# Kernel tuning notes

Hardware: AMD Instinct MI355X
Metric: run time of the kernel (lower is better)

The kernel has to match this reference:

```python
import jax, jax.numpy as jnp
import numpy as np


def setup_inputs() -> dict:
    key = jax.random.key(0)
    ks = jax.random.split(key, 8)
    B, H, W, C = 4, 64, 64, 64
    d = C // 8
    x = jax.random.normal(ks[0], (B, H, W, C), dtype=jnp.float32)
    # 1x1 conv kernels (spectral-normalized in the original; here we use the
    # already-normalized weight matrices directly, scaled to unit-ish norm)
    Wf = jax.random.normal(ks[1], (C, d), dtype=jnp.float32) * (1.0 / np.sqrt(C))
    bf = jnp.zeros((d,), dtype=jnp.float32)
    Wg = jax.random.normal(ks[2], (C, d), dtype=jnp.float32) * (1.0 / np.sqrt(C))
    bg = jnp.zeros((d,), dtype=jnp.float32)
    Wh = jax.random.normal(ks[3], (C, C), dtype=jnp.float32) * (1.0 / np.sqrt(C))
    bh = jnp.zeros((C,), dtype=jnp.float32)
    gamma = jnp.float32(1.0)
    return {"x": x, "Wf": Wf, "bf": bf, "Wg": Wg, "bg": bg,
            "Wh": Wh, "bh": bh, "gamma": gamma}


def reference(x, Wf, bf, Wg, bg, Wh, bh, gamma):
    # x: [B, H, W, C] (NHWC, as Keras Conv2D default)
    B, H, W, C = x.shape
    N = H * W
    # 1x1 convs == per-pixel channel matmuls
    q = jnp.einsum('bhwc,cd->bhwd', x, Wf) + bf   # [B,H,W,C//8]
    k = jnp.einsum('bhwc,cd->bhwd', x, Wg) + bg   # [B,H,W,C//8]
    v = jnp.einsum('bhwc,cd->bhwd', x, Wh) + bh   # [B,H,W,C]
    q = q.reshape(B, N, -1)
    k = k.reshape(B, N, -1)
    v = v.reshape(B, N, C)
    # full non-causal attention (no 1/sqrt(d) scaling in the original)
    s = jnp.einsum('bnd,bmd->bnm', q, k)          # [B,N,N]
    s = jax.nn.softmax(s, axis=-1)
    o = jnp.einsum('bnm,bmc->bnc', s, v)          # [B,N,C]
    o = o.reshape(B, H, W, C)
    return gamma * o + x
```

## Files before the change

### kernel.cpp

```cpp
#include <hip/hip_runtime.h>
#include <hip/hip_bf16.h>

#define BATCH 4
#define NTOK 4096
#define CCH 64
#define KSPLIT 2
#define KPB (NTOK / KSPLIT)
#define NTILE (KPB / 64)
#define TPW (NTILE / 4)

#define QSCALE 184.66496523f
#define SBIAS  16251.0f

typedef short s16x8 __attribute__((ext_vector_type(8)));
typedef float f32x4 __attribute__((ext_vector_type(4)));

static __device__ __forceinline__ unsigned short f2bf(float f) {
    union { __hip_bfloat16 h; unsigned short u; } cv;
    cv.h = __float2bfloat16(f);
    return cv.u;
}
static __device__ __forceinline__ float bf2f(unsigned short u) {
    union { unsigned int u; float f; } c; c.u = ((unsigned)u) << 16;
    return c.f;
}
static __device__ __forceinline__ float bf_split(float f, unsigned short& h) {
    h = f2bf(f);
    return f - bf2f(h);
}
static __device__ __forceinline__ unsigned pack_rne(float a, float b) {
    return ((unsigned)f2bf(b) << 16) | f2bf(a);
}
static __device__ __forceinline__ unsigned pack_bits(float a, float b) {
    return ((unsigned)(int)b << 16) | (unsigned)(int)a;
}

__global__ __launch_bounds__(256) void proj_kernel(
    const float* __restrict__ xg,
    const float* __restrict__ Wf, const float* __restrict__ bf_,
    const float* __restrict__ Wg, const float* __restrict__ bg,
    const float* __restrict__ Wh, const float* __restrict__ bh,
    unsigned short* __restrict__ Qp, unsigned short* __restrict__ Kp,
    unsigned short* __restrict__ vTg)
{
    __shared__ float xS[32 * 68];
    __shared__ unsigned short xbS[32 * 72];
    __shared__ float WfT[8 * 68];
    __shared__ float WgT[8 * 68];
    __shared__ unsigned short vtS[64 * 40];

    const int t = threadIdx.x;
    const int b = blockIdx.x >> 7;
    const int n0 = (blockIdx.x & 127) * 32;

    const float* xrow = xg + ((size_t)b * NTOK + n0) * CCH;
    for (int f = t; f < 512; f += 256) {
        int r = f >> 4, c4 = (f & 15) * 4;
        float4 v = *(const float4*)(xrow + r * 64 + c4);
        *(float4*)(xS + r * 68 + c4) = v;
        uint2 pk = { pack_rne(v.x, v.y), pack_rne(v.z, v.w) };
        *(uint2*)(xbS + r * 72 + c4) = pk;
    }
    for (int e = t; e < 512; e += 256) {
        int ci = e >> 3, j = e & 7;
        WfT[j * 68 + ci] = Wf[e];
        WgT[j * 68 + ci] = Wg[e];
    }
    __syncthreads();

    const int w = t >> 6, lane = t & 63, ml = lane & 15, quad = lane >> 4;

    {
        s16x8 a0, a1;
        #pragma unroll
        for (int j = 0; j < 8; ++j) {
            a0[j] = (short)f2bf(Wh[(quad * 8 + j) * 64 + w * 16 + ml]);
            a1[j] = (short)f2bf(Wh[(32 + quad * 8 + j) * 64 + w * 16 + ml]);
        }
        #pragma unroll
        for (int nf = 0; nf < 2; ++nf) {
            int tok = nf * 16 + ml;
            s16x8 b0 = *(const s16x8*)(xbS + tok * 72 + quad * 8);
            s16x8 b1 = *(const s16x8*)(xbS + tok * 72 + 32 + quad * 8);
            f32x4 cc = __builtin_amdgcn_mfma_f32_16x16x32_bf16(a0, b0, (f32x4){0.f,0.f,0.f,0.f}, 0, 0, 0);
            cc = __builtin_amdgcn_mfma_f32_16x16x32_bf16(a1, b1, cc, 0, 0, 0);
            #pragma unroll
            for (int reg = 0; reg < 4; ++reg) {
                int cout = w * 16 + quad * 4 + reg;
                vtS[cout * 40 + nf * 16 + ml] = f2bf(cc[reg] + bh[cout]);
            }
        }
    }

    {
        int r = t >> 3, j = t & 7;
        float q = bf_[j], k = bg[j];
        for (int ci = 0; ci < 64; ci += 4) {
            float4 x4 = *(const float4*)(xS + r * 68 + ci);
            float4 wf4 = *(const float4*)(WfT + j * 68 + ci);
            float4 wg4 = *(const float4*)(WgT + j * 68 + ci);
            q += x4.x * wf4.x + x4.y * wf4.y + x4.z * wf4.z + x4.w * wf4.w;
            k += x4.x * wg4.x + x4.y * wg4.y + x4.z * wg4.z + x4.w * wg4.w;
        }
        q *= QSCALE;
        unsigned short qh, kh;
        float qres = bf_split(q, qh);
        float kres = bf_split(k, kh);
        unsigned short ql = f2bf(qres), kl = f2bf(kres);
        size_t qbase = ((size_t)b * NTOK + n0 + r) * 32;
        Qp[qbase + j]      = qh;
        Qp[qbase + 8 + j]  = ql;
        Qp[qbase + 16 + j] = qh;
        Qp[qbase + 24 + j] = 0;
        size_t kbase = ((size_t)b * NTOK + n0 + r) * 16;
        Kp[kbase + j]     = kh;
        Kp[kbase + 8 + j] = kl;
    }
    __syncthreads();

    {
        int c_ = t >> 2, chunk = t & 3;
        uint4 v = *(const uint4*)(vtS + c_ * 40 + chunk * 8);
        *(uint4*)(vTg + ((size_t)b * CCH + c_) * NTOK + n0 + chunk * 8) = v;
    }
}

__global__ __launch_bounds__(256, 2) void attn_kernel(
    const unsigned short* __restrict__ Qp,
    const unsigned short* __restrict__ Kp,
    const unsigned short* __restrict__ vTg,
    unsigned short* __restrict__ Opart,
    float* __restrict__ lpart)
{
    __shared__ unsigned short KC[KPB * 16];

    const int t = threadIdx.x;
    const int blk = blockIdx.x;
    const int b = blk >> 7;
    const int qt = (blk >> 1) & 63;
    const int ks = blk & 1;
    const int m0 = qt * 64;
    const int kb0 = ks * KPB;
    const int w = t >> 6, lane = t & 63;
    const int ml = lane & 15, quad = lane >> 4;

    const unsigned short* qpb = Qp + (size_t)b * NTOK * 32;
    const unsigned short* kpb = Kp + (size_t)b * NTOK * 16;
    const unsigned short* vtb = vTg + (size_t)b * CCH * NTOK;

    for (int kk = t; kk < KPB; kk += 256) {
        const unsigned short* src = kpb + (size_t)(kb0 + kk) * 16;
        *(uint4*)(&KC[kk * 16])     = *(const uint4*)(src);
        *(uint4*)(&KC[kk * 16 + 8]) = *(const uint4*)(src + 8);
    }

    s16x8 qf[4];
    #pragma unroll
    for (int qg = 0; qg < 4; ++qg)
        qf[qg] = *(const s16x8*)(qpb + (size_t)(m0 + qg * 16 + ml) * 32 + quad * 8);

    const int keyA = 8 * (ml >> 2) + (ml & 3);
    const int khsel = (quad == 2) ? 8 : 0;

    s16x8 ones;
    #pragma unroll
    for (int i = 0; i < 8; ++i) ones[i] = (short)0x3F80;

    f32x4 o[4][4];
    f32x4 lac[4];
    #pragma unroll
    for (int cg = 0; cg < 4; ++cg)
        #pragma unroll
        for (int qg = 0; qg < 4; ++qg) o[cg][qg] = (f32x4){0.f,0.f,0.f,0.f};
    #pragma unroll
    for (int qg = 0; qg < 4; ++qg) lac[qg] = (f32x4){0.f,0.f,0.f,0.f};
    const f32x4 sb = {SBIAS, SBIAS, SBIAS, SBIAS};

    __syncthreads();

    const int tile0 = w * TPW;
    s16x8 kf0 = *(const s16x8*)(&KC[(tile0 * 64 + keyA) * 16 + khsel]);
    s16x8 kf1 = *(const s16x8*)(&KC[(tile0 * 64 + keyA + 4) * 16 + khsel]);
    s16x8 kf2 = *(const s16x8*)(&KC[(tile0 * 64 + 32 + keyA) * 16 + khsel]);
    s16x8 kf3 = *(const s16x8*)(&KC[(tile0 * 64 + 36 + keyA) * 16 + khsel]);

    for (int i = 0; i < TPW; ++i) {
        const int tile = w * TPW + i;
        const int kb = kb0 + tile * 64;

        s16x8 vf[4][2];
        #pragma unroll
        for (int cg = 0; cg < 4; ++cg) {
            const unsigned short* vr = vtb + (size_t)(cg * 16 + ml) * NTOK + kb + quad * 8;
            vf[cg][0] = *(const s16x8*)(vr);
            vf[cg][1] = *(const s16x8*)(vr + 32);
        }
        const int tn = (i + 1 < TPW) ? tile + 1 : tile0;
        s16x8 kn0 = *(const s16x8*)(&KC[(tn * 64 + keyA) * 16 + khsel]);
        s16x8 kn1 = *(const s16x8*)(&KC[(tn * 64 + keyA + 4) * 16 + khsel]);
        s16x8 kn2 = *(const s16x8*)(&KC[(tn * 64 + 32 + keyA) * 16 + khsel]);
        s16x8 kn3 = *(const s16x8*)(&KC[(tn * 64 + 36 + keyA) * 16 + khsel]);

        union { unsigned u[4]; s16x8 h; } P0[4], P1[4];
        #pragma unroll
        for (int qg = 0; qg < 4; ++qg) {
            f32x4 sA0 = __builtin_amdgcn_mfma_f32_16x16x32_bf16(kf0, qf[qg], sb, 0, 0, 0);
            f32x4 sB0 = __builtin_amdgcn_mfma_f32_16x16x32_bf16(kf1, qf[qg], sb, 0, 0, 0);
            f32x4 sA1 = __builtin_amdgcn_mfma_f32_16x16x32_bf16(kf2, qf[qg], sb, 0, 0, 0);
            f32x4 sB1 = __builtin_amdgcn_mfma_f32_16x16x32_bf16(kf3, qf[qg], sb, 0, 0, 0);
            P0[qg].u[0] = pack_bits(sA0[0], sA0[1]);
            P0[qg].u[1] = pack_bits(sA0[2], sA0[3]);
            P0[qg].u[2] = pack_bits(sB0[0], sB0[1]);
            P0[qg].u[3] = pack_bits(sB0[2], sB0[3]);
            P1[qg].u[0] = pack_bits(sA1[0], sA1[1]);
            P1[qg].u[1] = pack_bits(sA1[2], sA1[3]);
            P1[qg].u[2] = pack_bits(sB1[0], sB1[1]);
            P1[qg].u[3] = pack_bits(sB1[2], sB1[3]);
        }
        kf0 = kn0; kf1 = kn1; kf2 = kn2; kf3 = kn3;

        #pragma unroll
        for (int qg = 0; qg < 4; ++qg) {
            lac[qg] = __builtin_amdgcn_mfma_f32_16x16x32_bf16(ones, P0[qg].h, lac[qg], 0, 0, 0);
            lac[qg] = __builtin_amdgcn_mfma_f32_16x16x32_bf16(ones, P1[qg].h, lac[qg], 0, 0, 0);
        }
        #pragma unroll
        for (int cg = 0; cg < 4; ++cg)
            #pragma unroll
            for (int qg = 0; qg < 4; ++qg) {
                o[cg][qg] = __builtin_amdgcn_mfma_f32_16x16x32_bf16(vf[cg][0], P0[qg].h, o[cg][qg], 0, 0, 0);
                o[cg][qg] = __builtin_amdgcn_mfma_f32_16x16x32_bf16(vf[cg][1], P1[qg].h, o[cg][qg], 0, 0, 0);
            }
    }

    float* OL = (float*)KC;
    float* lL = OL + 64 * 68;
    #pragma unroll
    for (int r = 0; r < 4; ++r) {
        __syncthreads();
        if (w == r) {
            #pragma unroll
            for (int cg = 0; cg < 4; ++cg)
                #pragma unroll
                for (int qg = 0; qg < 4; ++qg) {
                    f32x4* p = (f32x4*)(&OL[(qg * 16 + ml) * 68 + cg * 16 + quad * 4]);
                    if (r == 0) *p = o[cg][qg];
                    else {
                        f32x4 v = *p;
                        v[0] += o[cg][qg][0]; v[1] += o[cg][qg][1];
                        v[2] += o[cg][qg][2]; v[3] += o[cg][qg][3];
                        *p = v;
                    }
                }
            if (quad == 0) {
                #pragma unroll
                for (int qg = 0; qg < 4; ++qg) {
                    if (r == 0) lL[qg * 16 + ml] = lac[qg][0];
                    else        lL[qg * 16 + ml] += lac[qg][0];
                }
            }
        }
    }
    __syncthreads();

    {
        int q = t >> 2, c0 = (t & 3) * 16;
        alignas(16) unsigned short us[16];
        #pragma unroll
        for (int k = 0; k < 16; ++k) us[k] = f2bf(OL[q * 68 + c0 + k]);
        size_t obase = ((size_t)ks * (BATCH * NTOK) + (size_t)b * NTOK + m0 + q) * 64 + c0;
        *(uint4*)(Opart + obase)     = *(uint4*)(us);
        *(uint4*)(Opart + obase + 8) = *(uint4*)(us + 8);
    }
    if (t < 64)
        lpart[ks * (BATCH * NTOK) + b * NTOK + m0 + t] = lL[t];
}

__global__ __launch_bounds__(256) void combine_kernel(
    const float* __restrict__ xg,
    const unsigned short* __restrict__ Opart,
    const float* __restrict__ lpart,
    const float* __restrict__ gammaPtr,
    float* __restrict__ out)
{
    const int i4 = blockIdx.x * 256 + threadIdx.x;
    const int base = i4 * 4;
    const int tok = base >> 6;

    float lsum = 0.f;
    #pragma unroll
    for (int s = 0; s < KSPLIT; ++s)
        lsum += lpart[s * (BATCH * NTOK) + tok];

    float o0 = 0.f, o1 = 0.f, o2 = 0.f, o3 = 0.f;
    #pragma unroll
    for (int s = 0; s < KSPLIT; ++s) {
        uint2 u = *(const uint2*)(Opart + (size_t)s * (BATCH * NTOK * 64) + base);
        o0 += bf2f((unsigned short)(u.x & 0xFFFF));
        o1 += bf2f((unsigned short)(u.x >> 16));
        o2 += bf2f((unsigned short)(u.y & 0xFFFF));
        o3 += bf2f((unsigned short)(u.y >> 16));
    }
    const float4 x4 = *(const float4*)(xg + base);
    const float gi = gammaPtr[0] / lsum;
    float4 r;
    r.x = gi * o0 + x4.x;
    r.y = gi * o1 + x4.y;
    r.z = gi * o2 + x4.z;
    r.w = gi * o3 + x4.w;
    *(float4*)(out + base) = r;
}

extern "C" void kernel_launch(void* const* d_in, const int* in_sizes, int n_in,
                              void* d_out, int out_size, void* d_ws, size_t ws_size,
                              hipStream_t stream) {
    const float* x  = (const float*)d_in[0];
    const float* Wf = (const float*)d_in[1];
    const float* bf = (const float*)d_in[2];
    const float* Wg = (const float*)d_in[3];
    const float* bg = (const float*)d_in[4];
    const float* Wh = (const float*)d_in[5];
    const float* bh = (const float*)d_in[6];
    const float* gamma = (const float*)d_in[7];
    float* out = (float*)d_out;

    char* ws = (char*)d_ws;
    unsigned short* Qp    = (unsigned short*)ws;
    unsigned short* Kp    = (unsigned short*)(ws + (1u << 20));
    unsigned short* vTg   = (unsigned short*)(ws + (2u << 20));
    unsigned short* Opart = (unsigned short*)(ws + (4u << 20));
    float*          lpart = (float*)(ws + (8u << 20));

    proj_kernel<<<BATCH * 128, 256, 0, stream>>>(x, Wf, bf, Wg, bg, Wh, bh,
                                                 Qp, Kp, vTg);
    attn_kernel<<<BATCH * 64 * KSPLIT, 256, 0, stream>>>(Qp, Kp, vTg, Opart, lpart);
    combine_kernel<<<(BATCH * NTOK * CCH) / 1024, 256, 0, stream>>>(x, Opart, lpart, gamma, out);
}
```

Baseline: 100.2 us.

## Fuse split-K combine into attention kernel via atomic last-block reduction

Removes the separate combine kernel launch. Each attention block bumps an atomic counter per (batch, query tile), and whichever of the two split-K blocks finishes second reads the other's partial O and row sum and writes the final gamma*o/l + x output. It uses its own fp32 OL from shared memory instead of a bf16 round trip. The counters are zeroed in the projection kernel. This saves a launch and an extra pass over the partials, at the cost of a threadfence, an atomic, and a serialized epilogue in half the blocks.

After: 159.4 us. +59.2%, slower.

```diff
diff --git a/kernel.cpp b/kernel.cpp
--- a/kernel.cpp
+++ b/kernel.cpp
@@ -41,7 +41,7 @@
     const float* __restrict__ Wg, const float* __restrict__ bg,
     const float* __restrict__ Wh, const float* __restrict__ bh,
     unsigned short* __restrict__ Qp, unsigned short* __restrict__ Kp,
-    unsigned short* __restrict__ vTg)
+    unsigned short* __restrict__ vTg, int* __restrict__ cnt)
 {
     __shared__ float xS[32 * 68];
     __shared__ unsigned short xbS[32 * 72];
@@ -52,6 +52,8 @@
     const int t = threadIdx.x;
     const int b = blockIdx.x >> 7;
     const int n0 = (blockIdx.x & 127) * 32;
+
+    if (blockIdx.x == 0 && t < BATCH * 64) cnt[t] = 0;
 
     const float* xrow = xg + ((size_t)b * NTOK + n0) * CCH;
     for (int f = t; f < 512; f += 256) {
@@ -126,13 +128,18 @@
 }
 
 __global__ __launch_bounds__(256, 2) void attn_kernel(
+    const float* __restrict__ xg,
     const unsigned short* __restrict__ Qp,
     const unsigned short* __restrict__ Kp,
     const unsigned short* __restrict__ vTg,
+    const float* __restrict__ gammaPtr,
     unsigned short* __restrict__ Opart,
-    float* __restrict__ lpart)
+    float* __restrict__ lpart,
+    int* __restrict__ cnt,
+    float* __restrict__ out)
 {
     __shared__ unsigned short KC[KPB * 16];
+    __shared__ int lastFlag;
 
     const int t = threadIdx.x;
     const int blk = blockIdx.x;
@@ -185,7 +192,7 @@
     s16x8 kf3 = *(const s16x8*)(&KC[(tile0 * 64 + 36 + keyA) * 16 + khsel]);
 
     for (int i = 0; i < TPW; ++i) {
-        const int tile = w * TPW + i;
+        const int tile = tile0 + i;
         const int kb = kb0 + tile * 64;
 
         s16x8 vf[4][2];
@@ -274,41 +281,35 @@
     }
     if (t < 64)
         lpart[ks * (BATCH * NTOK) + b * NTOK + m0 + t] = lL[t];
-}
-
-__global__ __launch_bounds__(256) void combine_kernel(
-    const float* __restrict__ xg,
-    const unsigned short* __restrict__ Opart,
-    const float* __restrict__ lpart,
-    const float* __restrict__ gammaPtr,
-    float* __restrict__ out)
-{
-    const int i4 = blockIdx.x * 256 + threadIdx.x;
-    const int base = i4 * 4;
-    const int tok = base >> 6;
-
-    float lsum = 0.f;
-    #pragma unroll
-    for (int s = 0; s < KSPLIT; ++s)
-        lsum += lpart[s * (BATCH * NTOK) + tok];
-
-    float o0 = 0.f, o1 = 0.f, o2 = 0.f, o3 = 0.f;
-    #pragma unroll
-    for (int s = 0; s < KSPLIT; ++s) {
-        uint2 u = *(const uint2*)(Opart + (size_t)s * (BATCH * NTOK * 64) + base);
-        o0 += bf2f((unsigned short)(u.x & 0xFFFF));
-        o1 += bf2f((unsigned short)(u.x >> 16));
-        o2 += bf2f((unsigned short)(u.y & 0xFFFF));
-        o3 += bf2f((unsigned short)(u.y >> 16));
-    }
-    const float4 x4 = *(const float4*)(xg + base);
-    const float gi = gammaPtr[0] / lsum;
-    float4 r;
-    r.x = gi * o0 + x4.x;
-    r.y = gi * o1 + x4.y;
-    r.z = gi * o2 + x4.z;
-    r.w = gi * o3 + x4.w;
-    *(float4*)(out + base) = r;
+
+    __threadfence();
+    if (t == 0) {
+        int old = atomicAdd(&cnt[b * 64 + qt], 1);
+        lastFlag = (old == 1);
+    }
+    __syncthreads();
+    if (lastFlag) {
+        const int os = ks ^ 1;
+        const float gamma = gammaPtr[0];
+        const int q = t >> 2, c0 = (t & 3) * 16;
+        const float lother =
+            *(volatile const float*)(lpart + os * (BATCH * NTOK) + b * NTOK + m0 + q);
+        const float gi = gamma / (lL[q] + lother);
+        size_t pb = ((size_t)os * (BATCH * NTOK) + (size_t)b * NTOK + m0 + q) * 64 + c0;
+        volatile const unsigned* op = (volatile const unsigned*)(Opart + pb);
+        size_t base = ((size_t)b * NTOK + m0 + q) * CCH + c0;
+        #pragma unroll
+        for (int u = 0; u < 8; ++u) {
+            unsigned pk = op[u];
+            float o0 = OL[q * 68 + c0 + u * 2 + 0] + bf2f((unsigned short)(pk & 0xFFFF));
+            float o1 = OL[q * 68 + c0 + u * 2 + 1] + bf2f((unsigned short)(pk >> 16));
+            float2 x2 = *(const float2*)(xg + base + u * 2);
+            float2 r;
+            r.x = gi * o0 + x2.x;
+            r.y = gi * o1 + x2.y;
+            *(float2*)(out + base + u * 2) = r;
+        }
+    }
 }
 
 extern "C" void kernel_launch(void* const* d_in, const int* in_sizes, int n_in,
@@ -330,9 +331,10 @@
     unsigned short* vTg   = (unsigned short*)(ws + (2u << 20));
     unsigned short* Opart = (unsigned short*)(ws + (4u << 20));
     float*          lpart = (float*)(ws + (8u << 20));
+    int*            cnt   = (int*)(ws + (9u << 20));
 
     proj_kernel<<<BATCH * 128, 256, 0, stream>>>(x, Wf, bf, Wg, bg, Wh, bh,
-                                                 Qp, Kp, vTg);
-    attn_kernel<<<BATCH * 64 * KSPLIT, 256, 0, stream>>>(Qp, Kp, vTg, Opart, lpart);
-    combine_kernel<<<(BATCH * NTOK * CCH) / 1024, 256, 0, stream>>>(x, Opart, lpart, gamma, out);
-}
+                                                 Qp, Kp, vTg, cnt);
+    attn_kernel<<<BATCH * 64 * KSPLIT, 256, 0, stream>>>(x, Qp, Kp, vTg, gamma,
+                                                         Opart, lpart, cnt, out);
+}
```
